# Performance work log

Hardware: AMD Instinct MI355X
Metric: run time of the kernel (lower is better)

## Reference

```python
import jax, jax.numpy as jnp
import numpy as np

N = 50000      # nodes
EPS = 1e-5     # BatchNorm eps


def setup_inputs() -> dict:
    key = jax.random.key(0)
    ks = jax.random.split(key, 8)
    F_IN, H, C, E = 128, 128, 40, 600000
    x = jax.random.normal(ks[0], (N, F_IN), jnp.float32)
    edge_index = jax.random.randint(ks[1], (2, E), 0, N, dtype=jnp.int64)
    def glorot(k, fi, fo):
        s = np.sqrt(6.0 / (fi + fo)).astype(np.float32)
        return jax.random.uniform(k, (fi, fo), jnp.float32, -s, s)
    return {
        "x": x, "edge_index": edge_index,
        "W1": glorot(ks[2], F_IN, H), "b1": jnp.zeros((H,), jnp.float32),
        "gamma1": jnp.ones((H,), jnp.float32), "beta1": jnp.zeros((H,), jnp.float32),
        "W2": glorot(ks[3], H, H), "b2": jnp.zeros((H,), jnp.float32),
        "gamma2": jnp.ones((H,), jnp.float32), "beta2": jnp.zeros((H,), jnp.float32),
        "W3": glorot(ks[4], H, C), "b3": jnp.zeros((C,), jnp.float32),
    }


def _gcn_conv(x, W, b, src, dst, norm):
    # X' = D^-1/2 (A+I) D^-1/2 (X W) + b   (PyG GCNConv with self-loops)
    h = x @ W                               # [N, Fo]
    msg = h[src] * norm[:, None]            # [E+N, Fo] gather + scale
    out = jax.ops.segment_sum(msg, dst, num_segments=N)  # scatter-add
    return out + b


def _batchnorm(x, gamma, beta):
    # training-mode BatchNorm1d: batch stats over node axis, biased variance
    mu = jnp.mean(x, axis=0)
    var = jnp.mean(jnp.square(x - mu), axis=0)
    return (x - mu) * jax.lax.rsqrt(var + EPS) * gamma + beta


def reference(x, edge_index, W1, b1, gamma1, beta1, W2, b2, gamma2, beta2, W3, b3):
    loops = jnp.arange(N, dtype=edge_index.dtype)
    src = jnp.concatenate([edge_index[0], loops])
    dst = jnp.concatenate([edge_index[1], loops])
    deg = jax.ops.segment_sum(jnp.ones_like(dst, dtype=x.dtype), dst, num_segments=N)
    dinv = jax.lax.rsqrt(jnp.maximum(deg, 1.0))  # deg >= 1 due to self-loops
    norm = dinv[src] * dinv[dst]                 # [E+N]

    h = _gcn_conv(x, W1, b1, src, dst, norm)
    h = jax.nn.relu(_batchnorm(h, gamma1, beta1))
    h = _gcn_conv(h, W2, b2, src, dst, norm)
    h = jax.nn.relu(_batchnorm(h, gamma2, beta2))
    h = _gcn_conv(h, W3, b3, src, dst, norm)
    return jax.nn.log_softmax(h, axis=-1)
```

## Files before the change

### kernel.cpp

```cpp
#include <hip/hip_runtime.h>
#include <hip/hip_bf16.h>

#define EPS 1e-5f
#define SCAN_BLOCKS 256

typedef __attribute__((ext_vector_type(8))) short bf16x8;
typedef __attribute__((ext_vector_type(4))) float f32x4;

__device__ inline float bf2f(unsigned short u) {
    union { unsigned int i; float f; } v;
    v.i = ((unsigned int)u) << 16;
    return v.f;
}

__device__ inline unsigned short f2bf(float f) {
    union { float f; unsigned int i; } v;
    v.f = f;
    unsigned int x = v.i;
    unsigned int rounded = x + 0x7FFF + ((x >> 16) & 1);
    return (unsigned short)(rounded >> 16);
}


__global__ void count_kernel(const int* __restrict__ dst, int* __restrict__ counts, int e) {
    int i = blockIdx.x * blockDim.x + threadIdx.x;
    if (i < e) atomicAdd(&counts[dst[i]], 1);
}

__global__ __launch_bounds__(256) void scan_partial_kernel(const int* __restrict__ counts,
                                                           int* __restrict__ partials, int n) {
    __shared__ int sh[256];
    int chunk = (n + gridDim.x - 1) / gridDim.x;
    int lo = blockIdx.x * chunk;
    int hi = lo + chunk; if (hi > n) hi = n;
    int s = 0;
    for (int i = lo + threadIdx.x; i < hi; i += 256) s += counts[i];
    sh[threadIdx.x] = s;
    __syncthreads();
    for (int d = 128; d; d >>= 1) {
        if (threadIdx.x < d) sh[threadIdx.x] += sh[threadIdx.x + d];
        __syncthreads();
    }
    if (threadIdx.x == 0) partials[blockIdx.x] = sh[0];
}

__global__ __launch_bounds__(256) void scan_level2_kernel(int* __restrict__ partials) {
    __shared__ int sh[256];
    int t = threadIdx.x;
    sh[t] = partials[t];
    __syncthreads();
    for (int d = 1; d < 256; d <<= 1) {
        int v = (t >= d) ? sh[t - d] : 0;
        __syncthreads();
        sh[t] += v;
        __syncthreads();
    }
    partials[t] = (t == 0) ? 0 : sh[t - 1];
}

__global__ __launch_bounds__(256) void scan_write_kernel(const int* __restrict__ counts,
                                                         const int* __restrict__ partials,
                                                         int* __restrict__ offs,
                                                         float* __restrict__ dinv, int n) {
    __shared__ int sh[256];
    int t = threadIdx.x;
    int chunk = (n + gridDim.x - 1) / gridDim.x;
    int lo = blockIdx.x * chunk;
    int hi = lo + chunk; if (hi > n) hi = n;
    int per = (chunk + 255) / 256;
    int tlo = lo + t * per;
    int thi = tlo + per; if (thi > hi) thi = hi;
    int s = 0;
    for (int i = tlo; i < thi; ++i) s += counts[i];
    sh[t] = s;
    __syncthreads();
    for (int d = 1; d < 256; d <<= 1) {
        int v = (t >= d) ? sh[t - d] : 0;
        __syncthreads();
        sh[t] += v;
        __syncthreads();
    }
    int run = partials[blockIdx.x] + ((t == 0) ? 0 : sh[t - 1]);
    for (int i = tlo; i < thi; ++i) {
        offs[i] = run;
        run += counts[i];
        dinv[i] = rsqrtf((float)(counts[i] + 1));
    }
    if (tlo < n && thi == n) offs[n] = run;
}

__global__ void scatter_kernel(const int* __restrict__ src, const int* __restrict__ dst,
                               const int* __restrict__ offs, int* __restrict__ fill,
                               const float* __restrict__ dinv,
                               int2* __restrict__ csr, int e) {
    int i = blockIdx.x * blockDim.x + threadIdx.x;
    if (i >= e) return;
    int s = src[i], d = dst[i];
    int pos = offs[d] + atomicAdd(&fill[d], 1);
    float w = dinv[s] * dinv[d];
    csr[pos] = make_int2(s, __float_as_int(w));
}

__global__ void prep_weights_kernel(const float* __restrict__ W1, const float* __restrict__ W2,
                                    const float* __restrict__ W3,
                                    unsigned short* __restrict__ WT1,
                                    unsigned short* __restrict__ WT2,
                                    unsigned short* __restrict__ WT3) {
    int i = blockIdx.x * blockDim.x + threadIdx.x;
    if (i < 16384) {
        int col = i >> 7, k = i & 127;
        WT1[i] = f2bf(W1[k * 128 + col]);
    } else if (i < 32768) {
        int j = i - 16384;
        int col = j >> 7, k = j & 127;
        WT2[j] = f2bf(W2[k * 128 + col]);
    } else if (i < 32768 + 6144) {
        int j = i - 32768;
        int col = j >> 7, k = j & 127;
        WT3[j] = (col < 40) ? f2bf(W3[k * 40 + col]) : 0;
    }
}

template<int MODE>
__global__ __launch_bounds__(256) void gemm128_mfma_kernel(
    const void* __restrict__ Aptr, const unsigned short* __restrict__ WT,
    const float* __restrict__ stats, const float* __restrict__ gamma,
    const float* __restrict__ beta, float invn,
    unsigned short* __restrict__ C, int n) {
    __shared__ unsigned short lW[128 * 128];
    __shared__ unsigned short lA[64 * 128];
    __shared__ float scs[128], shs[128];
    int tid = threadIdx.x;
    if (MODE == 1) {
        if (tid < 128) {
            float mu = stats[tid] * invn;
            float var = stats[128 + tid] * invn - mu * mu;
            float sc = gamma[tid] * rsqrtf(var + EPS);
            scs[tid] = sc;
            shs[tid] = beta[tid] - mu * sc;
        }
        __syncthreads();
    }
    const uint4* wsrc = (const uint4*)WT;
#pragma unroll
    for (int it = 0; it < 8; ++it) {
        int idx = tid + it * 256;
        int byte = idx << 4;
        int dst = byte ^ (((byte >> 8) & 7) << 4);
        *(uint4*)((char*)lW + dst) = wsrc[idx];
    }
    int row0 = blockIdx.x * 64;
#pragma unroll
    for (int it = 0; it < 4; ++it) {
        int idx = tid + it * 256;
        int r = idx >> 4;
        int cc = (idx & 15) << 3;
        int gr = row0 + r; if (gr > n - 1) gr = n - 1;
        union { unsigned short u[8]; uint4 q; } t;
        if (MODE == 0) {
            const float* ap = (const float*)Aptr + (size_t)gr * 128 + cc;
            float4 f0 = *(const float4*)ap;
            float4 f1 = *(const float4*)(ap + 4);
            float v[8] = {f0.x, f0.y, f0.z, f0.w, f1.x, f1.y, f1.z, f1.w};
#pragma unroll
            for (int j = 0; j < 8; ++j) t.u[j] = f2bf(v[j]);
        } else {
            uint4 q = *(const uint4*)((const unsigned short*)Aptr + (size_t)gr * 128 + cc);
            unsigned int w[4] = {q.x, q.y, q.z, q.w};
#pragma unroll
            for (int j = 0; j < 8; ++j) {
                float x = bf2f((unsigned short)(w[j >> 1] >> ((j & 1) * 16)));
                int c = cc + j;
                x = fmaf(x, scs[c], shs[c]);
                x = x > 0.0f ? x : 0.0f;
                t.u[j] = f2bf(x);
            }
        }
        int byte = idx << 4;
        int dst = byte ^ (((byte >> 8) & 7) << 4);
        *(uint4*)((char*)lA + dst) = t.q;
    }
    __syncthreads();

    int lane = tid & 63;
    int mrow0 = (tid >> 6) << 4;
    int arow = mrow0 + (lane & 15);
    int swz = (lane & 7) << 4;
    int koff = (lane >> 4) << 4;
    const char* pA = (const char*)lA + (arow << 8);
    const char* pB = (const char*)lW + ((lane & 15) << 8);
    f32x4 acc[8];
#pragma unroll
    for (int t8 = 0; t8 < 8; ++t8) acc[t8] = (f32x4){0.f, 0.f, 0.f, 0.f};
#pragma unroll
    for (int kk = 0; kk < 4; ++kk) {
        int kb = (kk << 6) + koff;
        bf16x8 af = *(const bf16x8*)(pA + (kb ^ swz));
#pragma unroll
        for (int t8 = 0; t8 < 8; ++t8) {
            bf16x8 bf = *(const bf16x8*)(pB + (t8 << 12) + (kb ^ swz));
            acc[t8] = __builtin_amdgcn_mfma_f32_16x16x32_bf16(af, bf, acc[t8], 0, 0, 0);
        }
    }
    int crow = row0 + mrow0 + ((lane >> 4) << 2);
    int ccol = lane & 15;
    unsigned short* cp = C + (size_t)crow * 128 + ccol;
#pragma unroll
    for (int j = 0; j < 4; ++j) {
        if (crow + j < n) {
#pragma unroll
            for (int t8 = 0; t8 < 8; ++t8)
                cp[(size_t)j * 128 + t8 * 16] = f2bf(acc[t8][j]);
        }
    }
}

__global__ __launch_bounds__(256) void gemm40_lsm_mfma_kernel(
    const unsigned short* __restrict__ A, const unsigned short* __restrict__ WT,
    const float* __restrict__ b3, float* __restrict__ out, int n) {
    __shared__ unsigned short lW[48 * 128];
    __shared__ unsigned short lA[64 * 128];
    __shared__ float sRow[64 * 49];
    __shared__ float sD[64];
    __shared__ float sB[48];
    int tid = threadIdx.x;
    if (tid < 48) sB[tid] = (tid < 40) ? b3[tid] : 0.0f;
    const uint4* wsrc = (const uint4*)WT;
#pragma unroll
    for (int it = 0; it < 3; ++it) {
        int idx = tid + it * 256;
        int byte = idx << 4;
        int dst = byte ^ (((byte >> 8) & 7) << 4);
        *(uint4*)((char*)lW + dst) = wsrc[idx];
    }
    int row0 = blockIdx.x * 64;
#pragma unroll
    for (int it = 0; it < 4; ++it) {
        int idx = tid + it * 256;
        int r = idx >> 4;
        int cc = (idx & 15) << 3;
        int gr = row0 + r; if (gr > n - 1) gr = n - 1;
        uint4 q = *(const uint4*)(A + (size_t)gr * 128 + cc);
        int byte = idx << 4;
        int dst = byte ^ (((byte >> 8) & 7) << 4);
        *(uint4*)((char*)lA + dst) = q;
    }
    __syncthreads();

    int lane = tid & 63;
    int mrow0 = (tid >> 6) << 4;
    int arow = mrow0 + (lane & 15);
    int swz = (lane & 7) << 4;
    int koff = (lane >> 4) << 4;
    const char* pA = (const char*)lA + (arow << 8);
    const char* pB = (const char*)lW + ((lane & 15) << 8);
    f32x4 acc[3];
#pragma unroll
    for (int t8 = 0; t8 < 3; ++t8) acc[t8] = (f32x4){0.f, 0.f, 0.f, 0.f};
#pragma unroll
    for (int kk = 0; kk < 4; ++kk) {
        int kb = (kk << 6) + koff;
        bf16x8 af = *(const bf16x8*)(pA + (kb ^ swz));
#pragma unroll
        for (int t8 = 0; t8 < 3; ++t8) {
            bf16x8 bf = *(const bf16x8*)(pB + (t8 << 12) + (kb ^ swz));
            acc[t8] = __builtin_amdgcn_mfma_f32_16x16x32_bf16(af, bf, acc[t8], 0, 0, 0);
        }
    }
    int lrow = mrow0 + ((lane >> 4) << 2);
    int ccol = lane & 15;
#pragma unroll
    for (int t8 = 0; t8 < 3; ++t8)
#pragma unroll
        for (int j = 0; j < 4; ++j)
            sRow[(lrow + j) * 49 + t8 * 16 + ccol] = acc[t8][j] + sB[t8 * 16 + ccol];
    __syncthreads();
    if (tid < 64) {
        float m = -1e30f;
        for (int c = 0; c < 40; ++c) m = fmaxf(m, sRow[tid * 49 + c]);
        float l = 0.0f;
        for (int c = 0; c < 40; ++c) l += expf(sRow[tid * 49 + c] - m);
        sD[tid] = m + logf(l);
    }
    __syncthreads();
    for (int i = tid; i < 64 * 40; i += 256) {
        int r = i / 40;
        int c = i - r * 40;
        int gr = row0 + r;
        if (gr < n) out[(size_t)gr * 40 + c] = sRow[r * 49 + c] - sD[r];
    }
}


template<bool BN>
__global__ __launch_bounds__(256) void aggregate128_kernel(
    const unsigned short* __restrict__ H, const int* __restrict__ offs,
    const int2* __restrict__ csr, const float* __restrict__ dinv,
    const float* __restrict__ stats, const float* __restrict__ gamma,
    const float* __restrict__ beta, float invn,
    unsigned short* __restrict__ out, int n) {
    int node = (blockIdx.x * blockDim.x + threadIdx.x) >> 6;
    if (node >= n) return;
    int lane = threadIdx.x & 63;
    int half = lane >> 5;
    int c0 = (lane & 31) * 4;
    float scv[4], shv[4];
    if (BN) {
#pragma unroll
        for (int j = 0; j < 4; ++j) {
            int c = c0 + j;
            float mu = stats[c] * invn;
            float var = stats[128 + c] * invn - mu * mu;
            scv[j] = gamma[c] * rsqrtf(var + EPS);
            shv[j] = beta[c] - mu * scv[j];
        }
    }
    auto loadf = [&](int row) -> float4 {
        uint2 hv = *(const uint2*)(H + (size_t)row * 128 + c0);
        float4 r;
        r.x = bf2f((unsigned short)hv.x);
        r.y = bf2f((unsigned short)(hv.x >> 16));
        r.z = bf2f((unsigned short)hv.y);
        r.w = bf2f((unsigned short)(hv.y >> 16));
        if (BN) {
            r.x = fmaf(r.x, scv[0], shv[0]); r.x = r.x > 0.0f ? r.x : 0.0f;
            r.y = fmaf(r.y, scv[1], shv[1]); r.y = r.y > 0.0f ? r.y : 0.0f;
            r.z = fmaf(r.z, scv[2], shv[2]); r.z = r.z > 0.0f ? r.z : 0.0f;
            r.w = fmaf(r.w, scv[3], shv[3]); r.w = r.w > 0.0f ? r.w : 0.0f;
        }
        return r;
    };
    float4 a0 = make_float4(0.f, 0.f, 0.f, 0.f);
    float4 a1 = a0, a2 = a0, a3 = a0;
    if (half == 0) {
        float di = dinv[node];
        float dd = di * di;
        float4 s = loadf(node);
        a0.x = s.x * dd; a0.y = s.y * dd; a0.z = s.z * dd; a0.w = s.w * dd;
    }
    int e = offs[node], e1 = offs[node + 1];
    for (; e + 8 <= e1; e += 8) {
        int2 q0 = csr[e + half];
        int2 q1 = csr[e + 2 + half];
        int2 q2 = csr[e + 4 + half];
        int2 q3 = csr[e + 6 + half];
        float4 h0 = loadf(q0.x);
        float4 h1 = loadf(q1.x);
        float4 h2 = loadf(q2.x);
        float4 h3 = loadf(q3.x);
        float w0 = __int_as_float(q0.y), w1 = __int_as_float(q1.y);
        float w2 = __int_as_float(q2.y), w3 = __int_as_float(q3.y);
        a0.x = fmaf(h0.x, w0, a0.x); a0.y = fmaf(h0.y, w0, a0.y);
        a0.z = fmaf(h0.z, w0, a0.z); a0.w = fmaf(h0.w, w0, a0.w);
        a1.x = fmaf(h1.x, w1, a1.x); a1.y = fmaf(h1.y, w1, a1.y);
        a1.z = fmaf(h1.z, w1, a1.z); a1.w = fmaf(h1.w, w1, a1.w);
        a2.x = fmaf(h2.x, w2, a2.x); a2.y = fmaf(h2.y, w2, a2.y);
        a2.z = fmaf(h2.z, w2, a2.z); a2.w = fmaf(h2.w, w2, a2.w);
        a3.x = fmaf(h3.x, w3, a3.x); a3.y = fmaf(h3.y, w3, a3.y);
        a3.z = fmaf(h3.z, w3, a3.z); a3.w = fmaf(h3.w, w3, a3.w);
    }
    for (; e + 2 <= e1; e += 2) {
        int2 q = csr[e + half];
        float4 h = loadf(q.x);
        float w = __int_as_float(q.y);
        a0.x = fmaf(h.x, w, a0.x); a0.y = fmaf(h.y, w, a0.y);
        a0.z = fmaf(h.z, w, a0.z); a0.w = fmaf(h.w, w, a0.w);
    }
    if (e < e1 && half == 0) {
        int2 q = csr[e];
        float4 h = loadf(q.x);
        float w = __int_as_float(q.y);
        a0.x = fmaf(h.x, w, a0.x); a0.y = fmaf(h.y, w, a0.y);
        a0.z = fmaf(h.z, w, a0.z); a0.w = fmaf(h.w, w, a0.w);
    }
    float4 acc;
    acc.x = (a0.x + a1.x) + (a2.x + a3.x);
    acc.y = (a0.y + a1.y) + (a2.y + a3.y);
    acc.z = (a0.z + a1.z) + (a2.z + a3.z);
    acc.w = (a0.w + a1.w) + (a2.w + a3.w);
    acc.x += __shfl_xor(acc.x, 32);
    acc.y += __shfl_xor(acc.y, 32);
    acc.z += __shfl_xor(acc.z, 32);
    acc.w += __shfl_xor(acc.w, 32);
    if (half == 0) {
        uint2 pack;
        pack.x = (unsigned int)f2bf(acc.x) | ((unsigned int)f2bf(acc.y) << 16);
        pack.y = (unsigned int)f2bf(acc.z) | ((unsigned int)f2bf(acc.w) << 16);
        *(uint2*)(out + (size_t)node * 128 + c0) = pack;
    }
}


__global__ __launch_bounds__(256) void bn_stats_kernel(const unsigned short* __restrict__ X,
                                                       float* __restrict__ stats, int n) {
    int tid = threadIdx.x;
    int c = tid & 127;
    int r0 = blockIdx.x * 2 + (tid >> 7);
    float s = 0.0f, q = 0.0f;
    for (int r = r0; r < n; r += gridDim.x * 2) {
        float v = bf2f(X[(size_t)r * 128 + c]);
        s += v;
        q += v * v;
    }
    __shared__ float sh[256], shq[256];
    sh[tid] = s; shq[tid] = q;
    __syncthreads();
    if (tid < 128) {
        atomicAdd(&stats[c], sh[tid] + sh[tid + 128]);
        atomicAdd(&stats[128 + c], shq[tid] + shq[tid + 128]);
    }
}


extern "C" void kernel_launch(void* const* d_in, const int* in_sizes, int n_in,
                              void* d_out, int out_size, void* d_ws, size_t ws_size,
                              hipStream_t stream) {
    const float* x   = (const float*)d_in[0];
    const int*   ei  = (const int*)d_in[1];
    const float* W1  = (const float*)d_in[2];
    const float* g1  = (const float*)d_in[4];
    const float* bt1 = (const float*)d_in[5];
    const float* W2  = (const float*)d_in[6];
    const float* g2  = (const float*)d_in[8];
    const float* bt2 = (const float*)d_in[9];
    const float* W3  = (const float*)d_in[10];
    const float* b3  = (const float*)d_in[11];

    int n = in_sizes[0] / 128;
    int e = in_sizes[1] / 2;
    const int* src = ei;
    const int* dst = ei + e;

    char* p = (char*)d_ws;
    auto alloc = [&](size_t bytes) -> char* {
        char* q = p;
        p += (bytes + 255) & ~(size_t)255;
        return q;
    };
    int*            counts   = (int*)alloc((size_t)n * 4);
    int*            offs     = (int*)alloc((size_t)(n + 1) * 4);
    int*            fill     = (int*)alloc((size_t)n * 4);
    float*          dinv     = (float*)alloc((size_t)n * 4);
    int*            partials = (int*)alloc(SCAN_BLOCKS * 4);
    int2*           csr      = (int2*)alloc((size_t)e * 8);
    float*          stats    = (float*)alloc(512 * 4);
    unsigned short* WT1      = (unsigned short*)alloc(16384 * 2);
    unsigned short* WT2      = (unsigned short*)alloc(16384 * 2);
    unsigned short* WT3      = (unsigned short*)alloc(6144 * 2);
    unsigned short* Hb       = (unsigned short*)alloc((size_t)n * 128 * 2);
    unsigned short* Ab       = (unsigned short*)alloc((size_t)n * 128 * 2);
    unsigned short* Ab2      = (unsigned short*)alloc((size_t)n * 128 * 2);
    unsigned short* Hb2      = (unsigned short*)alloc((size_t)n * 128 * 2);

    hipMemsetAsync(counts, 0, (size_t)n * 4, stream);
    hipMemsetAsync(fill, 0, (size_t)n * 4, stream);
    hipMemsetAsync(stats, 0, 512 * 4, stream);

    const int tb = 256;
    float invn = 1.0f / n;
    prep_weights_kernel<<<(38912 + tb - 1) / tb, tb, 0, stream>>>(W1, W2, W3, WT1, WT2, WT3);
    count_kernel<<<(e + tb - 1) / tb, tb, 0, stream>>>(dst, counts, e);
    scan_partial_kernel<<<SCAN_BLOCKS, tb, 0, stream>>>(counts, partials, n);
    scan_level2_kernel<<<1, tb, 0, stream>>>(partials);
    scan_write_kernel<<<SCAN_BLOCKS, tb, 0, stream>>>(counts, partials, offs, dinv, n);
    scatter_kernel<<<(e + tb - 1) / tb, tb, 0, stream>>>(src, dst, offs, fill, dinv, csr, e);

    int gblocks = (n + 63) / 64;
    int ablocks = (n + 3) / 4;

    gemm128_mfma_kernel<0><<<gblocks, tb, 0, stream>>>(x, WT1, nullptr, nullptr, nullptr,
                                                       0.0f, Hb, n);
    aggregate128_kernel<false><<<ablocks, tb, 0, stream>>>(Hb, offs, csr, dinv, nullptr,
                                                           nullptr, nullptr, 0.0f, Ab, n);
    bn_stats_kernel<<<256, tb, 0, stream>>>(Ab, stats, n);
    gemm128_mfma_kernel<1><<<gblocks, tb, 0, stream>>>(Ab, WT2, stats, g1, bt1, invn, Hb, n);
    aggregate128_kernel<false><<<ablocks, tb, 0, stream>>>(Hb, offs, csr, dinv, nullptr,
                                                           nullptr, nullptr, 0.0f, Ab2, n);
    bn_stats_kernel<<<256, tb, 0, stream>>>(Ab2, stats + 256, n);
    aggregate128_kernel<true><<<ablocks, tb, 0, stream>>>(Ab2, offs, csr, dinv, stats + 256,
                                                          g2, bt2, invn, Hb2, n);
    gemm40_lsm_mfma_kernel<<<gblocks, tb, 0, stream>>>(Hb2, WT3, b3, (float*)d_out, n);
}
```

Before: 274.0 us.

## Quantize gathered node features to int8 with per-row scales folded into edge weights

The GEMM outputs and the BN+ReLU layer-3 input are now stored as int8 with a per-row scale instead of bf16. This halves the bytes gathered per edge in the three aggregation passes. A prescale kernel multiplies each CSR edge weight by the source row's dequant scale, so aggregation does a plain int8-to-float FMA. The cost is three extra passes over the edge list, a separate BN-quantize pass, and a large loss of precision from 8-bit features, which may break accuracy tolerance.

```diff
diff --git a/kernel.cpp b/kernel.cpp
--- a/kernel.cpp
+++ b/kernel.cpp
@@ -99,6 +99,15 @@
     int pos = offs[d] + atomicAdd(&fill[d], 1);
     float w = dinv[s] * dinv[d];
     csr[pos] = make_int2(s, __float_as_int(w));
+}
+
+__global__ void prescale_kernel(const int2* __restrict__ csr, const float* __restrict__ scaleInv,
+                                int2* __restrict__ csrs, int e) {
+    int i = blockIdx.x * blockDim.x + threadIdx.x;
+    if (i >= e) return;
+    int2 q = csr[i];
+    float w = __int_as_float(q.y) * scaleInv[q.x];
+    csrs[i] = make_int2(q.x, __float_as_int(w));
 }
 
 __global__ void prep_weights_kernel(const float* __restrict__ W1, const float* __restrict__ W2,
@@ -126,7 +135,7 @@
     const void* __restrict__ Aptr, const unsigned short* __restrict__ WT,
     const float* __restrict__ stats, const float* __restrict__ gamma,
     const float* __restrict__ beta, float invn,
-    unsigned short* __restrict__ C, int n) {
+    signed char* __restrict__ Cq, float* __restrict__ scaleInv, int n) {
     __shared__ unsigned short lW[128 * 128];
     __shared__ unsigned short lA[64 * 128];
     __shared__ float scs[128], shs[128];
@@ -204,13 +213,28 @@
     }
     int crow = row0 + mrow0 + ((lane >> 4) << 2);
     int ccol = lane & 15;
-    unsigned short* cp = C + (size_t)crow * 128 + ccol;
+    float rmax[4];
+#pragma unroll
+    for (int j = 0; j < 4; ++j) {
+        float m = 0.0f;
+#pragma unroll
+        for (int t8 = 0; t8 < 8; ++t8) m = fmaxf(m, fabsf(acc[t8][j]));
+        rmax[j] = m;
+    }
+#pragma unroll
+    for (int d = 1; d < 16; d <<= 1) {
+#pragma unroll
+        for (int j = 0; j < 4; ++j) rmax[j] = fmaxf(rmax[j], __shfl_xor(rmax[j], d));
+    }
+    signed char* cp = Cq + (size_t)crow * 128 + ccol;
 #pragma unroll
     for (int j = 0; j < 4; ++j) {
         if (crow + j < n) {
+            float scale = rmax[j] > 0.0f ? 127.0f / rmax[j] : 0.0f;
+            if (ccol == 0) scaleInv[crow + j] = rmax[j] * (1.0f / 127.0f);
 #pragma unroll
             for (int t8 = 0; t8 < 8; ++t8)
-                cp[(size_t)j * 128 + t8 * 16] = f2bf(acc[t8][j]);
+                cp[(size_t)j * 128 + t8 * 16] = (signed char)__float2int_rn(acc[t8][j] * scale);
         }
     }
 }
@@ -292,86 +316,53 @@
 }
 
 
-template<bool BN>
-__global__ __launch_bounds__(256) void aggregate128_kernel(
-    const unsigned short* __restrict__ H, const int* __restrict__ offs,
-    const int2* __restrict__ csr, const float* __restrict__ dinv,
-    const float* __restrict__ stats, const float* __restrict__ gamma,
-    const float* __restrict__ beta, float invn,
-    unsigned short* __restrict__ out, int n) {
+__global__ __launch_bounds__(256) void aggregate128_q_kernel(
+    const signed char* __restrict__ Hq, const float* __restrict__ scaleInv,
+    const int* __restrict__ offs, const int2* __restrict__ csrs,
+    const float* __restrict__ dinv, unsigned short* __restrict__ out, int n) {
     int node = (blockIdx.x * blockDim.x + threadIdx.x) >> 6;
     if (node >= n) return;
     int lane = threadIdx.x & 63;
     int half = lane >> 5;
     int c0 = (lane & 31) * 4;
-    float scv[4], shv[4];
-    if (BN) {
-#pragma unroll
-        for (int j = 0; j < 4; ++j) {
-            int c = c0 + j;
-            float mu = stats[c] * invn;
-            float var = stats[128 + c] * invn - mu * mu;
-            scv[j] = gamma[c] * rsqrtf(var + EPS);
-            shv[j] = beta[c] - mu * scv[j];
-        }
-    }
-    auto loadf = [&](int row) -> float4 {
-        uint2 hv = *(const uint2*)(H + (size_t)row * 128 + c0);
-        float4 r;
-        r.x = bf2f((unsigned short)hv.x);
-        r.y = bf2f((unsigned short)(hv.x >> 16));
-        r.z = bf2f((unsigned short)hv.y);
-        r.w = bf2f((unsigned short)(hv.y >> 16));
-        if (BN) {
-            r.x = fmaf(r.x, scv[0], shv[0]); r.x = r.x > 0.0f ? r.x : 0.0f;
-            r.y = fmaf(r.y, scv[1], shv[1]); r.y = r.y > 0.0f ? r.y : 0.0f;
-            r.z = fmaf(r.z, scv[2], shv[2]); r.z = r.z > 0.0f ? r.z : 0.0f;
-            r.w = fmaf(r.w, scv[3], shv[3]); r.w = r.w > 0.0f ? r.w : 0.0f;
-        }
-        return r;
-    };
     float4 a0 = make_float4(0.f, 0.f, 0.f, 0.f);
     float4 a1 = a0, a2 = a0, a3 = a0;
+    auto fmaq = [&](float4& a, unsigned int qv, float w) {
+        a.x = fmaf((float)(signed char)(qv & 255), w, a.x);
+        a.y = fmaf((float)(signed char)((qv >> 8) & 255), w, a.y);
+        a.z = fmaf((float)(signed char)((qv >> 16) & 255), w, a.z);
+        a.w = fmaf((float)(signed char)(qv >> 24), w, a.w);
+    };
     if (half == 0) {
         float di = dinv[node];
-        float dd = di * di;
-        float4 s = loadf(node);
-        a0.x = s.x * dd; a0.y = s.y * dd; a0.z = s.z * dd; a0.w = s.w * dd;
+        float wd = di * di * scaleInv[node];
+        unsigned int hv = *(const unsigned int*)(Hq + (size_t)node * 128 + c0);
+        fmaq(a0, hv, wd);
     }
     int e = offs[node], e1 = offs[node + 1];
     for (; e + 8 <= e1; e += 8) {
-        int2 q0 = csr[e + half];
-        int2 q1 = csr[e + 2 + half];
-        int2 q2 = csr[e + 4 + half];
-        int2 q3 = csr[e + 6 + half];
-        float4 h0 = loadf(q0.x);
-        float4 h1 = loadf(q1.x);
-        float4 h2 = loadf(q2.x);
-        float4 h3 = loadf(q3.x);
-        float w0 = __int_as_float(q0.y), w1 = __int_as_float(q1.y);
-        float w2 = __int_as_float(q2.y), w3 = __int_as_float(q3.y);
-        a0.x = fmaf(h0.x, w0, a0.x); a0.y = fmaf(h0.y, w0, a0.y);
-        a0.z = fmaf(h0.z, w0, a0.z); a0.w = fmaf(h0.w, w0, a0.w);
-        a1.x = fmaf(h1.x, w1, a1.x); a1.y = fmaf(h1.y, w1, a1.y);
-        a1.z = fmaf(h1.z, w1, a1.z); a1.w = fmaf(h1.w, w1, a1.w);
-        a2.x = fmaf(h2.x, w2, a2.x); a2.y = fmaf(h2.y, w2, a2.y);
-        a2.z = fmaf(h2.z, w2, a2.z); a2.w = fmaf(h2.w, w2, a2.w);
-        a3.x = fmaf(h3.x, w3, a3.x); a3.y = fmaf(h3.y, w3, a3.y);
-        a3.z = fmaf(h3.z, w3, a3.z); a3.w = fmaf(h3.w, w3, a3.w);
+        int2 q0 = csrs[e + half];
+        int2 q1 = csrs[e + 2 + half];
+        int2 q2 = csrs[e + 4 + half];
+        int2 q3 = csrs[e + 6 + half];
+        unsigned int h0 = *(const unsigned int*)(Hq + (size_t)q0.x * 128 + c0);
+        unsigned int h1 = *(const unsigned int*)(Hq + (size_t)q1.x * 128 + c0);
+        unsigned int h2 = *(const unsigned int*)(Hq + (size_t)q2.x * 128 + c0);
+        unsigned int h3 = *(const unsigned int*)(Hq + (size_t)q3.x * 128 + c0);
+        fmaq(a0, h0, __int_as_float(q0.y));
+        fmaq(a1, h1, __int_as_float(q1.y));
+        fmaq(a2, h2, __int_as_float(q2.y));
+        fmaq(a3, h3, __int_as_float(q3.y));
     }
     for (; e + 2 <= e1; e += 2) {
-        int2 q = csr[e + half];
-        float4 h = loadf(q.x);
-        float w = __int_as_float(q.y);
-        a0.x = fmaf(h.x, w, a0.x); a0.y = fmaf(h.y, w, a0.y);
-        a0.z = fmaf(h.z, w, a0.z); a0.w = fmaf(h.w, w, a0.w);
+        int2 q = csrs[e + half];
+        unsigned int h = *(const unsigned int*)(Hq + (size_t)q.x * 128 + c0);
+        fmaq(a0, h, __int_as_float(q.y));
     }
     if (e < e1 && half == 0) {
-        int2 q = csr[e];
-        float4 h = loadf(q.x);
-        float w = __int_as_float(q.y);
-        a0.x = fmaf(h.x, w, a0.x); a0.y = fmaf(h.y, w, a0.y);
-        a0.z = fmaf(h.z, w, a0.z); a0.w = fmaf(h.w, w, a0.w);
+        int2 q = csrs[e];
+        unsigned int h = *(const unsigned int*)(Hq + (size_t)q.x * 128 + c0);
+        fmaq(a0, h, __int_as_float(q.y));
     }
     float4 acc;
     acc.x = (a0.x + a1.x) + (a2.x + a3.x);
@@ -411,6 +402,43 @@
     }
 }
 
+__global__ __launch_bounds__(256) void bnq_kernel(const unsigned short* __restrict__ X,
+                                                  const float* __restrict__ stats,
+                                                  const float* __restrict__ gamma,
+                                                  const float* __restrict__ beta, float invn,
+                                                  signed char* __restrict__ Y,
+                                                  float* __restrict__ scaleInv, int n) {
+    int wid = (blockIdx.x * blockDim.x + threadIdx.x) >> 6;
+    int lane = threadIdx.x & 63;
+    int nw = (gridDim.x * blockDim.x) >> 6;
+    int c0 = lane * 2;
+    float sc[2], sh[2];
+#pragma unroll
+    for (int j = 0; j < 2; ++j) {
+        int c = c0 + j;
+        float mu = stats[c] * invn;
+        float var = stats[128 + c] * invn - mu * mu;
+        sc[j] = gamma[c] * rsqrtf(var + EPS);
+        sh[j] = beta[c] - mu * sc[j];
+    }
+    for (int row = wid; row < n; row += nw) {
+        unsigned int v = *(const unsigned int*)(X + (size_t)row * 128 + c0);
+        float x0 = fmaf(bf2f((unsigned short)v), sc[0], sh[0]);
+        float x1 = fmaf(bf2f((unsigned short)(v >> 16)), sc[1], sh[1]);
+        x0 = x0 > 0.0f ? x0 : 0.0f;
+        x1 = x1 > 0.0f ? x1 : 0.0f;
+        float m = fmaxf(x0, x1);
+#pragma unroll
+        for (int d = 1; d < 64; d <<= 1) m = fmaxf(m, __shfl_xor(m, d));
+        float scale = m > 0.0f ? 127.0f / m : 0.0f;
+        int q0 = __float2int_rn(x0 * scale);
+        int q1 = __float2int_rn(x1 * scale);
+        unsigned short pk = (unsigned short)((q0 & 255) | ((q1 & 255) << 8));
+        *(unsigned short*)(Y + (size_t)row * 128 + c0) = pk;
+        if (lane == 0) scaleInv[row] = m * (1.0f / 127.0f);
+    }
+}
+
 
 extern "C" void kernel_launch(void* const* d_in, const int* in_sizes, int n_in,
                               void* d_out, int out_size, void* d_ws, size_t ws_size,
@@ -443,11 +471,13 @@
     float*          dinv     = (float*)alloc((size_t)n * 4);
     int*            partials = (int*)alloc(SCAN_BLOCKS * 4);
     int2*           csr      = (int2*)alloc((size_t)e * 8);
+    int2*           csrs     = (int2*)alloc((size_t)e * 8);
     float*          stats    = (float*)alloc(512 * 4);
     unsigned short* WT1      = (unsigned short*)alloc(16384 * 2);
     unsigned short* WT2      = (unsigned short*)alloc(16384 * 2);
     unsigned short* WT3      = (unsigned short*)alloc(6144 * 2);
-    unsigned short* Hb       = (unsigned short*)alloc((size_t)n * 128 * 2);
+    signed char*    Hq       = (signed char*)alloc((size_t)n * 128);
+    float*          scaleH   = (float*)alloc((size_t)n * 4);
     unsigned short* Ab       = (unsigned short*)alloc((size_t)n * 128 * 2);
     unsigned short* Ab2      = (unsigned short*)alloc((size_t)n * 128 * 2);
     unsigned short* Hb2      = (unsigned short*)alloc((size_t)n * 128 * 2);
@@ -467,17 +497,20 @@
 
     int gblocks = (n + 63) / 64;
     int ablocks = (n + 3) / 4;
-
-    gemm128_mfma_kernel<0><<<gblocks, tb, 0, stream>>>(x, WT1, nullptr, nullptr, nullptr,
-                                                       0.0f, Hb, n);
-    aggregate128_kernel<false><<<ablocks, tb, 0, stream>>>(Hb, offs, csr, dinv, nullptr,
-                                                           nullptr, nullptr, 0.0f, Ab, n);
+    int pblocks = (e + tb - 1) / tb;
+
+    gemm128_mfma_kernel<0><<<gblocks, tb, 0, stream>>>(x, WT1, nullptr, nullptr, nullptr, 0.0f,
+                                                       Hq, scaleH, n);
+    prescale_kernel<<<pblocks, tb, 0, stream>>>(csr, scaleH, csrs, e);
+    aggregate128_q_kernel<<<ablocks, tb, 0, stream>>>(Hq, scaleH, offs, csrs, dinv, Ab, n);
     bn_stats_kernel<<<256, tb, 0, stream>>>(Ab, stats, n);
-    gemm128_mfma_kernel<1><<<gblocks, tb, 0, stream>>>(Ab, WT2, stats, g1, bt1, invn, Hb, n);
-    aggregate128_kernel<false><<<ablocks, tb, 0, stream>>>(Hb, offs, csr, dinv, nullptr,
-                                                           nullptr, nullptr, 0.0f, Ab2, n);
+    gemm128_mfma_kernel<1><<<gblocks, tb, 0, stream>>>(Ab, WT2, stats, g1, bt1, invn,
+                                                       Hq, scaleH, n);
+    prescale_kernel<<<pblocks, tb, 0, stream>>>(csr, scaleH, csrs, e);
+    aggregate128_q_kernel<<<ablocks, tb, 0, stream>>>(Hq, scaleH, offs, csrs, dinv, Ab2, n);
     bn_stats_kernel<<<256, tb, 0, stream>>>(Ab2, stats + 256, n);
-    aggregate128_kernel<true><<<ablocks, tb, 0, stream>>>(Ab2, offs, csr, dinv, stats + 256,
-                                                          g2, bt2, invn, Hb2, n);
+    bnq_kernel<<<1024, tb, 0, stream>>>(Ab2, stats + 256, g2, bt2, invn, Hq, scaleH, n);
+    prescale_kernel<<<pblocks, tb, 0, stream>>>(csr, scaleH, csrs, e);
+    aggregate128_q_kernel<<<ablocks, tb, 0, stream>>>(Hq, scaleH, offs, csrs, dinv, Hb2, n);
     gemm40_lsm_mfma_kernel<<<gblocks, tb, 0, stream>>>(Hb2, WT3, b3, (float*)d_out, n);
 }
```

Result: slower. 283.4 us (+3.4%).
